# Performance work log

Hardware: AMD Instinct MI355X
Metric: run time of the kernel (lower is better)

The kernel has to match this reference:

```python
import jax, jax.numpy as jnp
import numpy as np

NUM_NODES = 100000
INPUT_DIM = 256
NUM_BAGS = 2048
BAG_SIZE = 64
N_EDGES = 3200000  # num_nodes * avg_degree(32)


def setup_inputs() -> dict:
    key = jax.random.key(0)
    ks = jax.random.split(key, 7)
    x = jax.random.normal(ks[0], (NUM_NODES, INPUT_DIM), dtype=jnp.float32)
    bags = jax.random.randint(ks[1], (NUM_BAGS, BAG_SIZE), 0, NUM_NODES)
    alpha_values = jax.random.uniform(ks[2], (NUM_BAGS, BAG_SIZE, 1), dtype=jnp.float32)
    # edge_dict in COO form: edge_src[e] has neighbor edge_nbr[e]
    edge_src = jax.random.randint(ks[3], (N_EDGES,), 0, NUM_NODES)
    edge_nbr = jax.random.randint(ks[4], (N_EDGES,), 0, NUM_NODES)
    node_weights = jax.random.uniform(ks[5], (NUM_NODES,), dtype=jnp.float32)  # torch.rand init
    theta_w = jax.random.normal(ks[6], (INPUT_DIM,), dtype=jnp.float32) / np.sqrt(INPUT_DIM)
    return dict(x=x, bags=bags, alpha_values=alpha_values, edge_src=edge_src,
                edge_nbr=edge_nbr, node_weights=node_weights, theta_w=theta_w)


def reference(x, bags, alpha_values, edge_src, edge_nbr, node_weights, theta_w):
    # Per-source neighbor weight sum: sum_value(source) = sum(node_weights[edge_dict[source]])
    nbr_sum = jax.ops.segment_sum(node_weights[edge_nbr], edge_src, num_segments=NUM_NODES)
    deg = jax.ops.segment_sum(jnp.ones_like(edge_src, dtype=x.dtype), edge_src,
                              num_segments=NUM_NODES)
    # sources not in edge_dict get sum_value = 1.0
    nbr_sum = jnp.where(deg > 0, nbr_sum, jnp.asarray(1.0, x.dtype))
    # h_values = theta(x[bag]); theta is Linear(input_dim, 1, bias=False)
    h = jnp.einsum('nbd,d->nb', x[bags], theta_w)          # [num_bags, bag_size]
    feat = h * alpha_values[..., 0]                         # [num_bags, bag_size]
    ns = nbr_sum[bags]                                      # [num_bags, bag_size]
    return jnp.sum(ns * feat, axis=1)                       # [num_bags]
```

## Files before the change

### kernel.cpp

```cpp
#include <hip/hip_runtime.h>

#define NUM_NODES 100000
#define INPUT_DIM 256
#define NUM_BAGS  2048
#define BAG_SIZE  64
#define N_EDGES   3200000
#define NQUAD     (N_EDGES / 4)
#define P_PART    8
#define NPP       12500
#define NSLICE    64

typedef unsigned int u32;

__global__ void __launch_bounds__(256)
pack_edges(const int* __restrict__ edge_src, const int* __restrict__ edge_nbr,
           const float* __restrict__ nw, u32* __restrict__ packed) {
    const int q = blockIdx.x * 256 + threadIdx.x;
    const int4 s4 = ((const int4*)edge_src)[q];
    const int4 n4 = ((const int4*)edge_nbr)[q];
#define PACK(S, N)  (((u32)(S) << 15) |                                     \
                     (((__float_as_uint(nw[(N)]) + 0x8000u) >> 16) & 0x7FFFu))
    uint4 o;
    o.x = PACK(s4.x, n4.x);
    o.y = PACK(s4.y, n4.y);
    o.z = PACK(s4.z, n4.z);
    o.w = PACK(s4.w, n4.w);
#undef PACK
    ((uint4*)packed)[q] = o;
}

__global__ void __launch_bounds__(1024)
hist_p(const u32* __restrict__ packed, float* __restrict__ rep) {
    __shared__ float hist[NPP];
    const int i    = blockIdx.x;
    const int r    = i & 7;
    const int p    = (i >> 3) & 7;
    const int b    = r | ((i >> 6) << 3);
    const int base = p * NPP;

    for (int j = threadIdx.x; j < NPP; j += 1024) hist[j] = 0.f;
    __syncthreads();

    const int per = NQUAD / NSLICE;
    const int lo  = b * per;
    const int hi  = lo + per;
    #pragma unroll 2
    for (int q = lo + (int)threadIdx.x; q < hi; q += 1024) {
        const uint4 w4 = ((const uint4*)packed)[q];
#define EDGE(W)                                                          \
        {                                                                \
            const u32 rel = ((W) >> 15) - (u32)base;                     \
            if (rel < (u32)NPP)                                          \
                atomicAdd(&hist[rel],                                    \
                          __uint_as_float(((W) & 0x7FFFu) << 16));       \
        }
        EDGE(w4.x)
        EDGE(w4.y)
        EDGE(w4.z)
        EDGE(w4.w)
#undef EDGE
    }
    __syncthreads();

    float* dst = rep + (size_t)b * NUM_NODES + base;
    for (int j = threadIdx.x; j < NPP; j += 1024)
        __builtin_nontemporal_store(hist[j], &dst[j]);
}

__global__ void __launch_bounds__(256)
reduce_rep(const float* __restrict__ rep, float* __restrict__ nbr_sum) {
    const int i = blockIdx.x * 256 + threadIdx.x;
    if (i >= NUM_NODES / 4) return;
    float4 a = make_float4(0.f, 0.f, 0.f, 0.f);
    #pragma unroll 8
    for (int r = 0; r < NSLICE; ++r) {
        const float4 v = ((const float4*)(rep + (size_t)r * NUM_NODES))[i];
        a.x += v.x; a.y += v.y; a.z += v.z; a.w += v.w;
    }
    float4 o;
    o.x = a.x > 0.f ? a.x : 1.0f;
    o.y = a.y > 0.f ? a.y : 1.0f;
    o.z = a.z > 0.f ? a.z : 1.0f;
    o.w = a.w > 0.f ? a.w : 1.0f;
    ((float4*)nbr_sum)[i] = o;
}

__global__ void __launch_bounds__(256)
gemv_h(const float* __restrict__ x, const float* __restrict__ theta,
       float* __restrict__ h) {
    const int lane = threadIdx.x & 63;
    const int wave = threadIdx.x >> 6;
    const float4 tw = *reinterpret_cast<const float4*>(&theta[lane * 4]);
    const int stride = gridDim.x * 4;
    for (int row = blockIdx.x * 4 + wave; row < NUM_NODES; row += stride) {
        const float4 xv =
            *reinterpret_cast<const float4*>(&x[(size_t)row * INPUT_DIM + lane * 4]);
        float d = xv.x * tw.x + xv.y * tw.y + xv.z * tw.z + xv.w * tw.w;
        #pragma unroll
        for (int off = 32; off >= 1; off >>= 1)
            d += __shfl_xor(d, off);
        if (lane == 0) h[row] = d;
    }
}

__global__ void __launch_bounds__(256)
bag_final(const int* __restrict__ bags, const float* __restrict__ alpha,
          const float* __restrict__ h, const float* __restrict__ ns,
          float* __restrict__ out) {
    const int bag  = blockIdx.x * 4 + (threadIdx.x >> 6);
    const int lane = threadIdx.x & 63;
    const int idx  = bags[bag * BAG_SIZE + lane];
    float v = h[idx] * ns[idx] * alpha[bag * BAG_SIZE + lane];
    #pragma unroll
    for (int off = 32; off >= 1; off >>= 1)
        v += __shfl_xor(v, off);
    if (lane == 0) out[bag] = v;
}

__global__ void __launch_bounds__(256)
edge_atomic(const int* __restrict__ edge_src, const int* __restrict__ edge_nbr,
            const float* __restrict__ nw, float* __restrict__ nbr_sum) {
    const int t = blockIdx.x * blockDim.x + threadIdx.x;
    const int4 s4 = ((const int4*)edge_src)[t];
    const int4 n4 = ((const int4*)edge_nbr)[t];
    atomicAdd(&nbr_sum[s4.x], nw[n4.x]);
    atomicAdd(&nbr_sum[s4.y], nw[n4.y]);
    atomicAdd(&nbr_sum[s4.z], nw[n4.z]);
    atomicAdd(&nbr_sum[s4.w], nw[n4.w]);
}

__global__ void __launch_bounds__(256)
fixup_nosum(float* __restrict__ nbr_sum) {
    const int i = blockIdx.x * 256 + threadIdx.x;
    if (i < NUM_NODES && nbr_sum[i] == 0.f) nbr_sum[i] = 1.0f;
}

extern "C" void kernel_launch(void* const* d_in, const int* in_sizes, int n_in,
                              void* d_out, int out_size, void* d_ws, size_t ws_size,
                              hipStream_t stream) {
    const float* x            = (const float*)d_in[0];
    const int*   bags         = (const int*)d_in[1];
    const float* alpha        = (const float*)d_in[2];
    const int*   edge_src     = (const int*)d_in[3];
    const int*   edge_nbr     = (const int*)d_in[4];
    const float* node_weights = (const float*)d_in[5];
    const float* theta        = (const float*)d_in[6];
    float*       out          = (float*)d_out;

    const size_t need_full =
        ((size_t)N_EDGES + (size_t)NSLICE * NUM_NODES + 2 * (size_t)NUM_NODES) * 4;

    if (ws_size >= need_full) {
        u32*   packed  = (u32*)d_ws;
        float* rep     = (float*)d_ws + N_EDGES;
        float* nbr_sum = rep + (size_t)NSLICE * NUM_NODES;
        float* h       = nbr_sum + NUM_NODES;

        pack_edges<<<NQUAD / 256, 256, 0, stream>>>(edge_src, edge_nbr,
                                                    node_weights, packed);
        hist_p<<<P_PART * NSLICE, 1024, 0, stream>>>(packed, rep);
        reduce_rep<<<(NUM_NODES / 4 + 255) / 256, 256, 0, stream>>>(rep, nbr_sum);
        gemv_h<<<2048, 256, 0, stream>>>(x, theta, h);
        bag_final<<<NUM_BAGS / 4, 256, 0, stream>>>(bags, alpha, h, nbr_sum, out);
    } else {
        float* nbr_sum = (float*)d_ws;
        float* h       = nbr_sum + NUM_NODES;
        hipMemsetAsync(nbr_sum, 0, (size_t)NUM_NODES * 4, stream);
        edge_atomic<<<(N_EDGES / 4) / 256, 256, 0, stream>>>(
            edge_src, edge_nbr, node_weights, nbr_sum);
        fixup_nosum<<<(NUM_NODES + 255) / 256, 256, 0, stream>>>(nbr_sum);
        gemv_h<<<2048, 256, 0, stream>>>(x, theta, h);
        bag_final<<<NUM_BAGS / 4, 256, 0, stream>>>(bags, alpha, h, nbr_sum, out);
    }
}
```

Before: 72.01 us.

## Halve histogram slices and fuse slice reduction with the theta GEMV launch

The number of per-slice partial histograms drops from 64 to 32. This halves both the slice buffer that is written and the reads the reduction must do, but each histogram block now processes twice as many edges and the grid shrinks to 256 blocks. The edge loop is unrolled explicitly with two 16-byte loads per iteration, and LDS clearing and the write-back now use float4 accesses. The slice reduction and the x·theta GEMV are merged into one launch, split by block index, so the small reduction overlaps the bandwidth-heavy GEMV and one launch gap is removed.

Result: faster. 66.92 us (-7.1%).

```diff
diff --git a/kernel.cpp b/kernel.cpp
--- a/kernel.cpp
+++ b/kernel.cpp
@@ -8,9 +8,11 @@
 #define NQUAD     (N_EDGES / 4)
 #define P_PART    8
 #define NPP       12500
-#define NSLICE    64
+#define NSLICE    32
+#define QPS       (NQUAD / NSLICE)
 
 typedef unsigned int u32;
+typedef float f4 __attribute__((ext_vector_type(4)));
 
 __global__ void __launch_bounds__(256)
 pack_edges(const int* __restrict__ edge_src, const int* __restrict__ edge_nbr,
@@ -38,15 +40,13 @@
     const int b    = r | ((i >> 6) << 3);
     const int base = p * NPP;
 
-    for (int j = threadIdx.x; j < NPP; j += 1024) hist[j] = 0.f;
+    for (int j = threadIdx.x; j < NPP / 4; j += 1024)
+        ((f4*)hist)[j] = (f4){0.f, 0.f, 0.f, 0.f};
     __syncthreads();
 
-    const int per = NQUAD / NSLICE;
-    const int lo  = b * per;
-    const int hi  = lo + per;
-    #pragma unroll 2
-    for (int q = lo + (int)threadIdx.x; q < hi; q += 1024) {
-        const uint4 w4 = ((const uint4*)packed)[q];
+    const int lo  = b * QPS;
+    const int tid = threadIdx.x;
+
 #define EDGE(W)                                                          \
         {                                                                \
             const u32 rel = ((W) >> 15) - (u32)base;                     \
@@ -54,35 +54,95 @@
                 atomicAdd(&hist[rel],                                    \
                           __uint_as_float(((W) & 0x7FFFu) << 16));       \
         }
-        EDGE(w4.x)
-        EDGE(w4.y)
-        EDGE(w4.z)
-        EDGE(w4.w)
+    #pragma unroll 2
+    for (int it = 0; it < 12; ++it) {
+        const int q0 = lo + it * 2048 + tid;
+        const uint4 a = ((const uint4*)packed)[q0];
+        const uint4 c = ((const uint4*)packed)[q0 + 1024];
+        EDGE(a.x) EDGE(a.y) EDGE(a.z) EDGE(a.w)
+        EDGE(c.x) EDGE(c.y) EDGE(c.z) EDGE(c.w)
+    }
+    if (tid < 424) {
+        const uint4 a = ((const uint4*)packed)[lo + 24576 + tid];
+        EDGE(a.x) EDGE(a.y) EDGE(a.z) EDGE(a.w)
+    }
 #undef EDGE
-    }
     __syncthreads();
 
     float* dst = rep + (size_t)b * NUM_NODES + base;
-    for (int j = threadIdx.x; j < NPP; j += 1024)
-        __builtin_nontemporal_store(hist[j], &dst[j]);
-}
-
-__global__ void __launch_bounds__(256)
-reduce_rep(const float* __restrict__ rep, float* __restrict__ nbr_sum) {
+    for (int j = threadIdx.x; j < NPP / 4; j += 1024) {
+        const f4 v = ((const f4*)hist)[j];
+        __builtin_nontemporal_store(v, &((f4*)dst)[j]);
+    }
+}
+
+#define RED_BLK 98
+__global__ void __launch_bounds__(256)
+gemv_reduce(const float* __restrict__ rep, float* __restrict__ nbr_sum,
+            const float* __restrict__ x, const float* __restrict__ theta,
+            float* __restrict__ h) {
+    if (blockIdx.x < RED_BLK) {
+        const int i = blockIdx.x * 256 + threadIdx.x;
+        if (i >= NUM_NODES / 4) return;
+        float4 a = make_float4(0.f, 0.f, 0.f, 0.f);
+        #pragma unroll 8
+        for (int r = 0; r < NSLICE; ++r) {
+            const float4 v = ((const float4*)(rep + (size_t)r * NUM_NODES))[i];
+            a.x += v.x; a.y += v.y; a.z += v.z; a.w += v.w;
+        }
+        float4 o;
+        o.x = a.x > 0.f ? a.x : 1.0f;
+        o.y = a.y > 0.f ? a.y : 1.0f;
+        o.z = a.z > 0.f ? a.z : 1.0f;
+        o.w = a.w > 0.f ? a.w : 1.0f;
+        ((float4*)nbr_sum)[i] = o;
+    } else {
+        const int gb   = blockIdx.x - RED_BLK;
+        const int lane = threadIdx.x & 63;
+        const int wave = threadIdx.x >> 6;
+        const float4 tw = *reinterpret_cast<const float4*>(&theta[lane * 4]);
+        for (int row = gb * 4 + wave; row < NUM_NODES; row += 2048 * 4) {
+            const float4 xv =
+                *reinterpret_cast<const float4*>(&x[(size_t)row * INPUT_DIM + lane * 4]);
+            float d = xv.x * tw.x + xv.y * tw.y + xv.z * tw.z + xv.w * tw.w;
+            #pragma unroll
+            for (int off = 32; off >= 1; off >>= 1)
+                d += __shfl_xor(d, off);
+            if (lane == 0) h[row] = d;
+        }
+    }
+}
+
+__global__ void __launch_bounds__(256)
+bag_final(const int* __restrict__ bags, const float* __restrict__ alpha,
+          const float* __restrict__ h, const float* __restrict__ ns,
+          float* __restrict__ out) {
+    const int bag  = blockIdx.x * 4 + (threadIdx.x >> 6);
+    const int lane = threadIdx.x & 63;
+    const int idx  = bags[bag * BAG_SIZE + lane];
+    float v = h[idx] * ns[idx] * alpha[bag * BAG_SIZE + lane];
+    #pragma unroll
+    for (int off = 32; off >= 1; off >>= 1)
+        v += __shfl_xor(v, off);
+    if (lane == 0) out[bag] = v;
+}
+
+__global__ void __launch_bounds__(256)
+edge_atomic(const int* __restrict__ edge_src, const int* __restrict__ edge_nbr,
+            const float* __restrict__ nw, float* __restrict__ nbr_sum) {
+    const int t = blockIdx.x * blockDim.x + threadIdx.x;
+    const int4 s4 = ((const int4*)edge_src)[t];
+    const int4 n4 = ((const int4*)edge_nbr)[t];
+    atomicAdd(&nbr_sum[s4.x], nw[n4.x]);
+    atomicAdd(&nbr_sum[s4.y], nw[n4.y]);
+    atomicAdd(&nbr_sum[s4.z], nw[n4.z]);
+    atomicAdd(&nbr_sum[s4.w], nw[n4.w]);
+}
+
+__global__ void __launch_bounds__(256)
+fixup_nosum(float* __restrict__ nbr_sum) {
     const int i = blockIdx.x * 256 + threadIdx.x;
-    if (i >= NUM_NODES / 4) return;
-    float4 a = make_float4(0.f, 0.f, 0.f, 0.f);
-    #pragma unroll 8
-    for (int r = 0; r < NSLICE; ++r) {
-        const float4 v = ((const float4*)(rep + (size_t)r * NUM_NODES))[i];
-        a.x += v.x; a.y += v.y; a.z += v.z; a.w += v.w;
-    }
-    float4 o;
-    o.x = a.x > 0.f ? a.x : 1.0f;
-    o.y = a.y > 0.f ? a.y : 1.0f;
-    o.z = a.z > 0.f ? a.z : 1.0f;
-    o.w = a.w > 0.f ? a.w : 1.0f;
-    ((float4*)nbr_sum)[i] = o;
+    if (i < NUM_NODES && nbr_sum[i] == 0.f) nbr_sum[i] = 1.0f;
 }
 
 __global__ void __launch_bounds__(256)
@@ -103,38 +163,6 @@
     }
 }
 
-__global__ void __launch_bounds__(256)
-bag_final(const int* __restrict__ bags, const float* __restrict__ alpha,
-          const float* __restrict__ h, const float* __restrict__ ns,
-          float* __restrict__ out) {
-    const int bag  = blockIdx.x * 4 + (threadIdx.x >> 6);
-    const int lane = threadIdx.x & 63;
-    const int idx  = bags[bag * BAG_SIZE + lane];
-    float v = h[idx] * ns[idx] * alpha[bag * BAG_SIZE + lane];
-    #pragma unroll
-    for (int off = 32; off >= 1; off >>= 1)
-        v += __shfl_xor(v, off);
-    if (lane == 0) out[bag] = v;
-}
-
-__global__ void __launch_bounds__(256)
-edge_atomic(const int* __restrict__ edge_src, const int* __restrict__ edge_nbr,
-            const float* __restrict__ nw, float* __restrict__ nbr_sum) {
-    const int t = blockIdx.x * blockDim.x + threadIdx.x;
-    const int4 s4 = ((const int4*)edge_src)[t];
-    const int4 n4 = ((const int4*)edge_nbr)[t];
-    atomicAdd(&nbr_sum[s4.x], nw[n4.x]);
-    atomicAdd(&nbr_sum[s4.y], nw[n4.y]);
-    atomicAdd(&nbr_sum[s4.z], nw[n4.z]);
-    atomicAdd(&nbr_sum[s4.w], nw[n4.w]);
-}
-
-__global__ void __launch_bounds__(256)
-fixup_nosum(float* __restrict__ nbr_sum) {
-    const int i = blockIdx.x * 256 + threadIdx.x;
-    if (i < NUM_NODES && nbr_sum[i] == 0.f) nbr_sum[i] = 1.0f;
-}
-
 extern "C" void kernel_launch(void* const* d_in, const int* in_sizes, int n_in,
                               void* d_out, int out_size, void* d_ws, size_t ws_size,
                               hipStream_t stream) {
@@ -159,8 +187,7 @@
         pack_edges<<<NQUAD / 256, 256, 0, stream>>>(edge_src, edge_nbr,
                                                     node_weights, packed);
         hist_p<<<P_PART * NSLICE, 1024, 0, stream>>>(packed, rep);
-        reduce_rep<<<(NUM_NODES / 4 + 255) / 256, 256, 0, stream>>>(rep, nbr_sum);
-        gemv_h<<<2048, 256, 0, stream>>>(x, theta, h);
+        gemv_reduce<<<RED_BLK + 2048, 256, 0, stream>>>(rep, nbr_sum, x, theta, h);
         bag_final<<<NUM_BAGS / 4, 256, 0, stream>>>(bags, alpha, h, nbr_sum, out);
     } else {
         float* nbr_sum = (float*)d_ws;
```

## Replace replicated histogram with bucket sort of packed edges by source

Applied to the files above, without the earlier changes.

Replaces the 64-way replicated partitioned shared-memory histogram and its reduction with a counting sort: edges are packed and counted into 391 buckets of 256 source nodes, offsets are computed with a scan, edges are scattered into bucket order, then each block builds a small shared histogram for its bucket. This removes the 64x NUM_NODES replica writes and the reduction pass, and avoids each block filtering all edges. In exchange it adds extra passes (count, two offset kernels, scatter with random global writes) and more launches.

New measurement: 90.79 us. 1.26x slower.

```diff
diff --git a/kernel.cpp b/kernel.cpp
--- a/kernel.cpp
+++ b/kernel.cpp
@@ -6,83 +6,129 @@
 #define BAG_SIZE  64
 #define N_EDGES   3200000
 #define NQUAD     (N_EDGES / 4)
-#define P_PART    8
-#define NPP       12500
-#define NSLICE    64
+#define NBKT      391
+#define BLK_A     256
+#define QPB       (NQUAD / BLK_A)
 
 typedef unsigned int u32;
 
-__global__ void __launch_bounds__(256)
-pack_edges(const int* __restrict__ edge_src, const int* __restrict__ edge_nbr,
-           const float* __restrict__ nw, u32* __restrict__ packed) {
-    const int q = blockIdx.x * 256 + threadIdx.x;
-    const int4 s4 = ((const int4*)edge_src)[q];
-    const int4 n4 = ((const int4*)edge_nbr)[q];
+__global__ void __launch_bounds__(1024)
+pack_count(const int* __restrict__ edge_src, const int* __restrict__ edge_nbr,
+           const float* __restrict__ nw, u32* __restrict__ packed,
+           u32* __restrict__ cnt) {
+    __shared__ u32 lcnt[NBKT];
+    const int blk = blockIdx.x;
+    const int tid = threadIdx.x;
+    for (int j = tid; j < NBKT; j += 1024) lcnt[j] = 0;
+    __syncthreads();
+
+    const int lo = blk * QPB, hi = lo + QPB;
+    for (int q = lo + tid; q < hi; q += 1024) {
+        const int4 s4 = ((const int4*)edge_src)[q];
+        const int4 n4 = ((const int4*)edge_nbr)[q];
 #define PACK(S, N)  (((u32)(S) << 15) |                                     \
                      (((__float_as_uint(nw[(N)]) + 0x8000u) >> 16) & 0x7FFFu))
-    uint4 o;
-    o.x = PACK(s4.x, n4.x);
-    o.y = PACK(s4.y, n4.y);
-    o.z = PACK(s4.z, n4.z);
-    o.w = PACK(s4.w, n4.w);
+        uint4 o;
+        o.x = PACK(s4.x, n4.x);
+        o.y = PACK(s4.y, n4.y);
+        o.z = PACK(s4.z, n4.z);
+        o.w = PACK(s4.w, n4.w);
 #undef PACK
-    ((uint4*)packed)[q] = o;
+        ((uint4*)packed)[q] = o;
+        atomicAdd(&lcnt[o.x >> 23], 1u);
+        atomicAdd(&lcnt[o.y >> 23], 1u);
+        atomicAdd(&lcnt[o.z >> 23], 1u);
+        atomicAdd(&lcnt[o.w >> 23], 1u);
+    }
+    __syncthreads();
+    for (int j = tid; j < NBKT; j += 1024) cnt[j * BLK_A + blk] = lcnt[j];
+}
+
+__global__ void __launch_bounds__(256)
+bucket_tot(const u32* __restrict__ cnt, u32* __restrict__ tot) {
+    __shared__ u32 s[256];
+    const int b = blockIdx.x;
+    s[threadIdx.x] = cnt[b * BLK_A + threadIdx.x];
+    __syncthreads();
+    for (int off = 128; off >= 1; off >>= 1) {
+        if (threadIdx.x < off) s[threadIdx.x] += s[threadIdx.x + off];
+        __syncthreads();
+    }
+    if (threadIdx.x == 0) tot[b] = s[0];
+}
+
+__global__ void __launch_bounds__(256)
+bucket_ofs(const u32* __restrict__ cnt, const u32* __restrict__ tot,
+           u32* __restrict__ gofs) {
+    __shared__ u32 s[256];
+    __shared__ u32 pb[256];
+    const int b   = blockIdx.x;
+    const int tid = threadIdx.x;
+
+    u32 part = 0;
+    if (tid < b) part += tot[tid];
+    if (tid + 256 < b) part += tot[tid + 256];
+    pb[tid] = part;
+    __syncthreads();
+    for (int off = 128; off >= 1; off >>= 1) {
+        if (tid < off) pb[tid] += pb[tid + off];
+        __syncthreads();
+    }
+    const u32 base = pb[0];
+
+    const u32 v = cnt[b * BLK_A + tid];
+    s[tid] = v;
+    for (int off = 1; off < 256; off <<= 1) {
+        __syncthreads();
+        const u32 t = (tid >= off) ? s[tid - off] : 0u;
+        __syncthreads();
+        s[tid] += t;
+    }
+    gofs[b * BLK_A + tid] = base + s[tid] - v;
 }
 
 __global__ void __launch_bounds__(1024)
-hist_p(const u32* __restrict__ packed, float* __restrict__ rep) {
-    __shared__ float hist[NPP];
-    const int i    = blockIdx.x;
-    const int r    = i & 7;
-    const int p    = (i >> 3) & 7;
-    const int b    = r | ((i >> 6) << 3);
-    const int base = p * NPP;
-
-    for (int j = threadIdx.x; j < NPP; j += 1024) hist[j] = 0.f;
-    __syncthreads();
-
-    const int per = NQUAD / NSLICE;
-    const int lo  = b * per;
-    const int hi  = lo + per;
-    #pragma unroll 2
-    for (int q = lo + (int)threadIdx.x; q < hi; q += 1024) {
-        const uint4 w4 = ((const uint4*)packed)[q];
-#define EDGE(W)                                                          \
-        {                                                                \
-            const u32 rel = ((W) >> 15) - (u32)base;                     \
-            if (rel < (u32)NPP)                                          \
-                atomicAdd(&hist[rel],                                    \
-                          __uint_as_float(((W) & 0x7FFFu) << 16));       \
+scatter(const u32* __restrict__ packed, const u32* __restrict__ gofs,
+        u32* __restrict__ sorted) {
+    __shared__ u32 cursor[NBKT];
+    const int blk = blockIdx.x;
+    const int tid = threadIdx.x;
+    for (int j = tid; j < NBKT; j += 1024) cursor[j] = gofs[j * BLK_A + blk];
+    __syncthreads();
+
+    const int lo = blk * QPB, hi = lo + QPB;
+    for (int q = lo + tid; q < hi; q += 1024) {
+        const uint4 o = ((const uint4*)packed)[q];
+#define PUT(W) { const u32 pos = atomicAdd(&cursor[(W) >> 23], 1u); sorted[pos] = (W); }
+        PUT(o.x) PUT(o.y) PUT(o.z) PUT(o.w)
+#undef PUT
+    }
+}
+
+__global__ void __launch_bounds__(512)
+bucket_hist(const u32* __restrict__ sorted, const u32* __restrict__ gofs,
+            float* __restrict__ nbr_sum) {
+    __shared__ float hist[256];
+    const int b   = blockIdx.x;
+    const int tid = threadIdx.x;
+    if (tid < 256) hist[tid] = 0.f;
+    __syncthreads();
+
+    const u32 lo = gofs[b * BLK_A + 0];
+    const u32 hi = (b + 1 < NBKT) ? gofs[(b + 1) * BLK_A + 0] : (u32)N_EDGES;
+    for (u32 i = lo + tid; i < hi; i += 512) {
+        const u32 w = sorted[i];
+        atomicAdd(&hist[(w >> 15) & 255u], __uint_as_float((w & 0x7FFFu) << 16));
+    }
+    __syncthreads();
+
+    if (tid < 256) {
+        const int n = b * 256 + tid;
+        if (n < NUM_NODES) {
+            const float s = hist[tid];
+            nbr_sum[n] = s > 0.f ? s : 1.0f;
         }
-        EDGE(w4.x)
-        EDGE(w4.y)
-        EDGE(w4.z)
-        EDGE(w4.w)
-#undef EDGE
-    }
-    __syncthreads();
-
-    float* dst = rep + (size_t)b * NUM_NODES + base;
-    for (int j = threadIdx.x; j < NPP; j += 1024)
-        __builtin_nontemporal_store(hist[j], &dst[j]);
-}
-
-__global__ void __launch_bounds__(256)
-reduce_rep(const float* __restrict__ rep, float* __restrict__ nbr_sum) {
-    const int i = blockIdx.x * 256 + threadIdx.x;
-    if (i >= NUM_NODES / 4) return;
-    float4 a = make_float4(0.f, 0.f, 0.f, 0.f);
-    #pragma unroll 8
-    for (int r = 0; r < NSLICE; ++r) {
-        const float4 v = ((const float4*)(rep + (size_t)r * NUM_NODES))[i];
-        a.x += v.x; a.y += v.y; a.z += v.z; a.w += v.w;
-    }
-    float4 o;
-    o.x = a.x > 0.f ? a.x : 1.0f;
-    o.y = a.y > 0.f ? a.y : 1.0f;
-    o.z = a.z > 0.f ? a.z : 1.0f;
-    o.w = a.w > 0.f ? a.w : 1.0f;
-    ((float4*)nbr_sum)[i] = o;
+    }
 }
 
 __global__ void __launch_bounds__(256)
@@ -148,18 +194,24 @@
     float*       out          = (float*)d_out;
 
     const size_t need_full =
-        ((size_t)N_EDGES + (size_t)NSLICE * NUM_NODES + 2 * (size_t)NUM_NODES) * 4;
+        ((size_t)N_EDGES * 2 + 2 * (size_t)NBKT * BLK_A + NBKT
+         + 2 * (size_t)NUM_NODES) * 4;
 
     if (ws_size >= need_full) {
         u32*   packed  = (u32*)d_ws;
-        float* rep     = (float*)d_ws + N_EDGES;
-        float* nbr_sum = rep + (size_t)NSLICE * NUM_NODES;
+        u32*   sorted  = packed + N_EDGES;
+        u32*   cnt     = sorted + N_EDGES;
+        u32*   gofs    = cnt + (size_t)NBKT * BLK_A;
+        u32*   tot     = gofs + (size_t)NBKT * BLK_A;
+        float* nbr_sum = (float*)(tot + NBKT);
         float* h       = nbr_sum + NUM_NODES;
 
-        pack_edges<<<NQUAD / 256, 256, 0, stream>>>(edge_src, edge_nbr,
-                                                    node_weights, packed);
-        hist_p<<<P_PART * NSLICE, 1024, 0, stream>>>(packed, rep);
-        reduce_rep<<<(NUM_NODES / 4 + 255) / 256, 256, 0, stream>>>(rep, nbr_sum);
+        pack_count<<<BLK_A, 1024, 0, stream>>>(edge_src, edge_nbr,
+                                               node_weights, packed, cnt);
+        bucket_tot<<<NBKT, 256, 0, stream>>>(cnt, tot);
+        bucket_ofs<<<NBKT, 256, 0, stream>>>(cnt, tot, gofs);
+        scatter<<<BLK_A, 1024, 0, stream>>>(packed, gofs, sorted);
+        bucket_hist<<<NBKT, 512, 0, stream>>>(sorted, gofs, nbr_sum);
         gemv_h<<<2048, 256, 0, stream>>>(x, theta, h);
         bag_final<<<NUM_BAGS / 4, 256, 0, stream>>>(bags, alpha, h, nbr_sum, out);
     } else {
```
